# Performance work log

Measured on AMD Instinct MI355X. Metric: run time of the kernel, lower is better.

Reference implementation:

```python
import jax, jax.numpy as jnp
import numpy as np

B, N, E, H = 256, 128, 256, 256
C_CLIP = 10.0


def setup_inputs() -> dict:
    key = jax.random.key(0)
    ks = jax.random.split(key, 12)
    u = lambda k, shape, b: jax.random.uniform(k, shape, jnp.float32, -b, b)
    return {
        "low_context_vector": jax.random.normal(ks[0], (B, N, E), jnp.float32),
        "original_node": jax.random.uniform(ks[1], (B, N, 2), jnp.float32),
        "mask": jnp.zeros((B, N), jnp.int32),
        "id": 0,
        "low_init_w": u(ks[2], (2 * E,), 1.0),                      # uniform_(-1, 1)
        "W_hbar": u(ks[3], (E, E), 1.0 / np.sqrt(E)),
        "b_hbar": u(ks[4], (E,), 1.0 / np.sqrt(E)),
        "W_rest": u(ks[5], (2 * E, E), 1.0 / np.sqrt(2 * E)),
        "b_rest": u(ks[6], (E,), 1.0 / np.sqrt(2 * E)),
        "W_k": u(ks[7], (E, H), 1.0 / np.sqrt(E)),
        "b_k": u(ks[8], (H,), 1.0 / np.sqrt(E)),
        "W_q": u(ks[9], (E, H), 1.0 / np.sqrt(E)),
        "b_q": u(ks[10], (H,), 1.0 / np.sqrt(E)),
        "v": u(ks[11], (H,), 1.0 / np.sqrt(H)),
    }


def reference(low_context_vector, original_node, mask, id,
              low_init_w, W_hbar, b_hbar, W_rest, b_rest,
              W_k, b_k, W_q, b_q, v):
    lcv = low_context_vector
    b, n, e = lcv.shape
    barange = jnp.arange(b)
    # target side of the pointer is fixed across steps -> precompute keys
    keys = lcv @ W_k + b_k                                   # [B, N, H]
    h_bar = jnp.mean(lcv, axis=1) @ W_hbar + b_hbar          # [B, E]
    query0 = h_bar + (low_init_w @ W_rest + b_rest)          # [B, E] (broadcast)
    step_keys = jax.random.split(jax.random.key(42), n)

    def step(carry, xs):
        query, msk, init_h, cur_idx = carry
        i, k = xs
        q = query @ W_q + b_q                                # [B, H]
        u = jnp.tanh(keys + q[:, None, :]) @ v               # [B, N]
        logits = C_CLIP * jnp.tanh(u)
        logits = jnp.where(msk == 1, -jnp.inf, logits)       # masked_fill
        idx = jax.random.categorical(k, logits)              # Categorical sample
        idx = jnp.where((i == 0) & (id == 0), jnp.zeros_like(idx), idx)
        logp = jax.nn.log_softmax(logits)[barange, idx]      # [B]
        msk = msk.at[barange, idx].set(1)                    # Environment.update_state
        h = lcv[barange, idx]                                # gather current node emb
        init_h = jnp.where(i == 0, h, init_h)
        query = h_bar + (jnp.concatenate([init_h, h], axis=-1) @ W_rest + b_rest)
        cur = original_node[barange, cur_idx]                # [B, 2]
        nxt = original_node[barange, idx]
        r = jnp.linalg.norm(nxt - cur, axis=-1)              # [B]
        return (query, msk, init_h, idx), (logp, idx, r)

    carry0 = (query0, mask, jnp.zeros((b, e), lcv.dtype), jnp.zeros((b,), jnp.int64))
    (_, _, _, last_idx), (logps, idxs, rs) = jax.lax.scan(
        step, carry0, (jnp.arange(n), step_keys))
    init_node = original_node[:, :1, :]                      # current_idx starts at 0
    last_node = original_node[barange, last_idx][:, None, :]
    return (logps.T, idxs.T, init_node, last_node, rs.T)
```

## Files before the change

kernel.cpp:

```cpp
#include <hip/hip_runtime.h>
#include <stdint.h>
#include <math.h>

#define NN 128
#define EE 256
#define HH 256

#define OFF_LOGP 0
#define OFF_IDX  32768
#define OFF_INIT 65536
#define OFF_LAST 66048
#define OFF_RS   66560

#define KST  260
#define KST4 65

__device__ __forceinline__ uint32_t rotl32_(uint32_t x, int d){ return (x<<d)|(x>>(32-d)); }

__device__ __forceinline__ void tf2x32(uint32_t k0, uint32_t k1, uint32_t x0, uint32_t x1,
                                       uint32_t& o0, uint32_t& o1){
  uint32_t k2 = k0 ^ k1 ^ 0x1BD11BDAu;
  x0 += k0; x1 += k1;
#define TF_RND(r) { x0 += x1; x1 = rotl32_(x1,(r)); x1 ^= x0; }
  TF_RND(13) TF_RND(15) TF_RND(26) TF_RND(6)
  x0 += k1; x1 += k2 + 1u;
  TF_RND(17) TF_RND(29) TF_RND(16) TF_RND(24)
  x0 += k2; x1 += k0 + 2u;
  TF_RND(13) TF_RND(15) TF_RND(26) TF_RND(6)
  x0 += k0; x1 += k1 + 3u;
  TF_RND(17) TF_RND(29) TF_RND(16) TF_RND(24)
  x0 += k1; x1 += k2 + 4u;
  TF_RND(13) TF_RND(15) TF_RND(26) TF_RND(6)
  x0 += k2; x1 += k0 + 5u;
#undef TF_RND
  o0 = x0; o1 = x1;
}

__device__ __forceinline__ float fast_tanhf(float x){
  float ax = __builtin_fabsf(x);
  float E = __builtin_amdgcn_exp2f(ax * -2.885390081777927f);
  float num = 1.0f - E;
  float den = 1.0f + E;
  float inv = __builtin_amdgcn_rcpf(den);
  inv = fmaf(fmaf(-den, inv, 1.0f), inv, inv);
  float r = num * inv;
  r = fmaf(fmaf(-den, r, num), inv, r);
  return __builtin_copysignf(r, x);
}

__device__ __forceinline__ float tanh_pre(float xs){
  float E = __builtin_amdgcn_exp2f(xs);
  return fmaf(-2.0f, __builtin_amdgcn_rcpf(1.0f + E), 1.0f);
}

__device__ __forceinline__ float jax_gumbel(uint32_t k0, uint32_t k1, uint32_t t){
  uint32_t o0, o1, bits;
  tf2x32(k0, k1, 0u, t, o0, o1);
  bits = o0 ^ o1;
  float u = __uint_as_float((bits >> 9) | 0x3f800000u) - 1.0f;
  const float kTiny = 1.17549435e-38f;
  u = fmaxf(kTiny, u + kTiny);
  return -logf(-logf(u));
}

#define CMB_DPP(CTRL) { \
  float ny_ = __int_as_float(__builtin_amdgcn_mov_dpp(__float_as_int(y), (CTRL), 0xf, 0xf, false)); \
  int   nj_ = __builtin_amdgcn_mov_dpp(pj, (CTRL), 0xf, 0xf, false); \
  float ne_ = __int_as_float(__builtin_amdgcn_mov_dpp(__float_as_int(es), (CTRL), 0xf, 0xf, false)); \
  es += ne_; \
  if (ny_ > y || (ny_ == y && nj_ < pj)){ y = ny_; pj = nj_; } }
#define CMB_SWZ16() { \
  float ny_ = __int_as_float(__builtin_amdgcn_ds_swizzle(__float_as_int(y), 0x401F)); \
  int   nj_ = __builtin_amdgcn_ds_swizzle(pj, 0x401F); \
  float ne_ = __int_as_float(__builtin_amdgcn_ds_swizzle(__float_as_int(es), 0x401F)); \
  es += ne_; \
  if (ny_ > y || (ny_ == y && nj_ < pj)){ y = ny_; pj = nj_; } }
#define CMB_SHF32() { \
  float ny_ = __shfl_xor(y, 32); \
  int   nj_ = __shfl_xor(pj, 32); \
  float ne_ = __shfl_xor(es, 32); \
  es += ne_; \
  if (ny_ > y || (ny_ == y && nj_ < pj)){ y = ny_; pj = nj_; } }

__global__ __launch_bounds__(256) void k_pre(
    const float* __restrict__ liw, const float* __restrict__ Wr,
    const float* __restrict__ Wq, const float* __restrict__ lcv,
    const float* __restrict__ Whbar, const float* __restrict__ bhbar,
    const float* __restrict__ brest, const float* __restrict__ bq,
    float* __restrict__ c0, float* __restrict__ T1, float* __restrict__ base)
{
  __shared__ float sbuf[512];
  const int bid = blockIdx.x;
  const int t = threadIdx.x;
  if (bid == 0){
    float acc = 0.f;
    for (int k = 0; k < 2*EE; ++k) acc = fmaf(liw[k], Wr[(size_t)k*EE + t], acc);
    sbuf[t] = acc;
    __syncthreads();
    float c = 0.f;
    for (int e = 0; e < EE; ++e) c = fmaf(sbuf[e], Wq[(size_t)e*HH + t], c);
    c0[t] = c;
  } else if (bid <= 512){
    const int r = bid - 1;
    float acc = 0.f;
    for (int e = 0; e < EE; ++e) acc = fmaf(Wr[(size_t)r*EE + e], Wq[(size_t)e*HH + t], acc);
    T1[(size_t)r*HH + t] = acc;
  } else {
    const int b = bid - 513;
    float* sm  = sbuf;
    float* hb2 = sbuf + 256;
    float acc = 0.f;
    const float* p = lcv + (size_t)b*NN*EE + t;
    for (int n = 0; n < NN; ++n) acc += p[(size_t)n*EE];
    sm[t] = acc * 0.0078125f;
    __syncthreads();
    float a2 = 0.f;
    for (int e = 0; e < EE; ++e) a2 = fmaf(sm[e], Whbar[(size_t)e*EE + t], a2);
    hb2[t] = (a2 + bhbar[t]) + brest[t];
    __syncthreads();
    float a3 = 0.f;
    for (int e = 0; e < EE; ++e) a3 = fmaf(hb2[e], Wq[(size_t)e*HH + t], a3);
    base[(size_t)b*HH + t] = a3 + bq[t];
  }
}

__global__ __launch_bounds__(1024) void k_keysP2(
    const float* __restrict__ lcv, const float* __restrict__ Wk,
    const float* __restrict__ T1, const float* __restrict__ bk,
    const float* __restrict__ base, const float* __restrict__ c0,
    const float* __restrict__ vvec,
    float* __restrict__ keysg, float* __restrict__ P2g, float* __restrict__ ltab)
{
  const int b = blockIdx.x, tid = threadIdx.x, wid = tid >> 6, lane = tid & 63;
  __shared__ __align__(16) float sbuf[20992];
  __shared__ __align__(16) float q0s[EE];
  __shared__ __align__(16) float vs[EE];
  float* sA = sbuf;
  float* sW = sbuf + 4608;
  float* sT = sbuf + 12800;
  if (tid < 64){
    float4 bs = ((const float4*)(base + (size_t)b*HH))[tid];
    const float4 cc = ((const float4*)c0)[tid];
    bs.x += cc.x; bs.y += cc.y; bs.z += cc.z; bs.w += cc.w;
    ((float4*)q0s)[tid] = bs;
    ((float4*)vs)[tid]  = ((const float4*)vvec)[tid];
  }
  float4 kacc[8], p2acc[8];
  #pragma unroll
  for (int r = 0; r < 8; ++r){
    kacc[r]  = make_float4(0.f,0.f,0.f,0.f);
    p2acc[r] = make_float4(0.f,0.f,0.f,0.f);
  }
  for (int ch = 0; ch < 8; ++ch){
    const int e0 = ch << 5;
    __syncthreads();
    {
      const int r = tid >> 3, c = tid & 7;
      const float4 t = ((const float4*)(lcv + ((size_t)b*NN + r)*EE + e0))[c];
      ((float4*)sA)[r*9 + c] = t;
    }
    #pragma unroll
    for (int s = 0; s < 2; ++s){
      const int idx4 = s*1024 + tid;
      const int e = idx4 >> 6, c = idx4 & 63;
      ((float4*)sW)[idx4] = ((const float4*)(Wk + (size_t)(e0+e)*HH))[c];
      ((float4*)sT)[idx4] = ((const float4*)(T1 + (size_t)(EE+e0+e)*HH))[c];
    }
    __syncthreads();
    const float* aRow = sA + (wid << 3)*36;
    for (int e = 0; e < 32; ++e){
      const float4 wv = ((const float4*)sW)[(e<<6) + lane];
      const float4 tv = ((const float4*)sT)[(e<<6) + lane];
      #pragma unroll
      for (int r = 0; r < 8; ++r){
        const float av = aRow[r*36 + e];
        kacc[r].x = fmaf(av, wv.x, kacc[r].x);
        kacc[r].y = fmaf(av, wv.y, kacc[r].y);
        kacc[r].z = fmaf(av, wv.z, kacc[r].z);
        kacc[r].w = fmaf(av, wv.w, kacc[r].w);
        p2acc[r].x = fmaf(av, tv.x, p2acc[r].x);
        p2acc[r].y = fmaf(av, tv.y, p2acc[r].y);
        p2acc[r].z = fmaf(av, tv.z, p2acc[r].z);
        p2acc[r].w = fmaf(av, tv.w, p2acc[r].w);
      }
    }
  }
  const float4 bkv = ((const float4*)bk)[lane];
  const float4 qv0 = ((const float4*)q0s)[lane];
  const float4 vv0 = ((const float4*)vs)[lane];
  #pragma unroll
  for (int r = 0; r < 8; ++r){
    const int j = (wid << 3) + r;
    float4 kv = kacc[r];
    kv.x += bkv.x; kv.y += bkv.y; kv.z += bkv.z; kv.w += bkv.w;
    ((float4*)(keysg + ((size_t)b*NN + j)*EE))[lane] = kv;
    ((float4*)(P2g   + ((size_t)b*NN + j)*EE))[lane] = p2acc[r];
    float p = 0.f;
    p = fmaf(fast_tanhf(kv.x + qv0.x), vv0.x, p);
    p = fmaf(fast_tanhf(kv.y + qv0.y), vv0.y, p);
    p = fmaf(fast_tanhf(kv.z + qv0.z), vv0.z, p);
    p = fmaf(fast_tanhf(kv.w + qv0.w), vv0.w, p);
    #pragma unroll
    for (int off = 1; off < 64; off <<= 1) p += __shfl_xor(p, off);
    if (lane == 0) ltab[((size_t)b*129 + 128)*NN + j] = 10.0f * fast_tanhf(p);
  }
}

__global__ __launch_bounds__(256) void k_idx0qb(
    const float* __restrict__ ltab, const int* __restrict__ mask_in,
    const int* __restrict__ id_in, const float* __restrict__ lcv,
    const float* __restrict__ T1, const float* __restrict__ base,
    float* __restrict__ qb)
{
  const int b = blockIdx.x, t = threadIdx.x, lane = t & 63;
  __shared__ int idx_sh;
  if (t < 64){
    const float NEG_INF = -__builtin_huge_valf();
    float l0 = ltab[((size_t)b*129 + 128)*NN + lane];
    float l1 = ltab[((size_t)b*129 + 128)*NN + 64 + lane];
    if (mask_in[(size_t)b*NN + lane])      l0 = NEG_INF;
    if (mask_in[(size_t)b*NN + 64 + lane]) l1 = NEG_INF;
    uint32_t k0, k1; tf2x32(0u, 42u, 0u, 0u, k0, k1);
    const float g0 = jax_gumbel(k0, k1, (uint32_t)(b*NN + lane));
    const float g1 = jax_gumbel(k0, k1, (uint32_t)(b*NN + 64 + lane));
    float y = l0 + g0; int pj = lane;
    { float yb = l1 + g1; if (yb > y){ y = yb; pj = 64 + lane; } }
    float es = 0.f;
    CMB_DPP(0xB1); CMB_DPP(0x4E); CMB_DPP(0x124); CMB_DPP(0x128);
    CMB_SWZ16(); CMB_SHF32();
    int bi = pj;
    if (id_in[0] == 0) bi = 0;
    if (lane == 0) idx_sh = bi;
  }
  __syncthreads();
  const int i0 = idx_sh;
  const float* arow = lcv + ((size_t)b*NN + i0)*EE;
  float acc = 0.f;
  #pragma unroll 4
  for (int e = 0; e < EE; ++e) acc = fmaf(arow[e], T1[(size_t)e*HH + t], acc);
  qb[(size_t)b*HH + t] = base[(size_t)b*HH + t] + acc;
}

__global__ __launch_bounds__(256) void k_tab(
    const float* __restrict__ keysg, const float* __restrict__ P2g,
    const float* __restrict__ qb, const float* __restrict__ vvec,
    float* __restrict__ l_tab)
{
  const int b  = blockIdx.x >> 2;
  const int jt = blockIdx.x & 3;
  const int t = threadIdx.x;
  const float CSC = 2.885390081777927f;
  __shared__ __align__(16) float skeys[32*65*4];
  __shared__ __align__(16) float sQ2[32*65*4];
  __shared__ __align__(16) float sv[EE];
  __shared__ __align__(16) float sqbc[EE];

  #pragma unroll
  for (int k = 0; k < 8; ++k){
    const int idx4 = t + 256*k;
    const int row = idx4 >> 6, hc = idx4 & 63;
    float4 kv = ((const float4*)(keysg + ((size_t)b*NN + jt*32 + row)*EE))[hc];
    kv.x *= CSC; kv.y *= CSC; kv.z *= CSC; kv.w *= CSC;
    ((float4*)skeys)[row*65 + (hc ^ ((row >> 2) & 7))] = kv;
  }
  if (t < 64){
    ((float4*)sv)[t]  = ((const float4*)vvec)[t];
    float4 qv = ((const float4*)(qb + (size_t)b*HH))[t];
    qv.x *= CSC; qv.y *= CSC; qv.z *= CSC; qv.w *= CSC;
    ((float4*)sqbc)[t] = qv;
  }
  const int jq = t & 7;
  const int iq = t >> 3;

  float4 pr[8];
  #pragma unroll
  for (int k = 0; k < 8; ++k){
    const int idx4 = t + 256*k;
    const int row = idx4 >> 6, hc = idx4 & 63;
    pr[k] = ((const float4*)(P2g + ((size_t)b*NN + row)*EE))[hc];
  }

  for (int ib = 0; ib < 4; ++ib){
    __syncthreads();
    #pragma unroll
    for (int k = 0; k < 8; ++k){
      const int idx4 = t + 256*k;
      const int row = idx4 >> 6, hc = idx4 & 63;
      const float4 qv = ((const float4*)sqbc)[hc];
      float4 pv;
      pv.x = fmaf(pr[k].x, CSC, qv.x);
      pv.y = fmaf(pr[k].y, CSC, qv.y);
      pv.z = fmaf(pr[k].z, CSC, qv.z);
      pv.w = fmaf(pr[k].w, CSC, qv.w);
      ((float4*)sQ2)[row*65 + hc] = pv;
    }
    if (ib + 1 < 4){
      #pragma unroll
      for (int k = 0; k < 8; ++k){
        const int idx4 = t + 256*k;
        const int row = idx4 >> 6, hc = idx4 & 63;
        pr[k] = ((const float4*)(P2g + ((size_t)b*NN + (ib+1)*32 + row)*EE))[hc];
      }
    }
    __syncthreads();
    float a0 = 0.f, a1 = 0.f, a2 = 0.f, a3 = 0.f;
    #pragma unroll 2
    for (int hc = 0; hc < 64; ++hc){
      const float4 qv = ((const float4*)sQ2)[iq*65 + hc];
      const float4 vv = ((const float4*)sv)[hc];
      const int hx = hc ^ jq;
      const float4 k0 = ((const float4*)skeys)[(jq*4 + 0)*65 + hx];
      const float4 k1 = ((const float4*)skeys)[(jq*4 + 1)*65 + hx];
      const float4 k2 = ((const float4*)skeys)[(jq*4 + 2)*65 + hx];
      const float4 k3 = ((const float4*)skeys)[(jq*4 + 3)*65 + hx];
      a0 = fmaf(tanh_pre(k0.x + qv.x), vv.x, a0);
      a0 = fmaf(tanh_pre(k0.y + qv.y), vv.y, a0);
      a0 = fmaf(tanh_pre(k0.z + qv.z), vv.z, a0);
      a0 = fmaf(tanh_pre(k0.w + qv.w), vv.w, a0);
      a1 = fmaf(tanh_pre(k1.x + qv.x), vv.x, a1);
      a1 = fmaf(tanh_pre(k1.y + qv.y), vv.y, a1);
      a1 = fmaf(tanh_pre(k1.z + qv.z), vv.z, a1);
      a1 = fmaf(tanh_pre(k1.w + qv.w), vv.w, a1);
      a2 = fmaf(tanh_pre(k2.x + qv.x), vv.x, a2);
      a2 = fmaf(tanh_pre(k2.y + qv.y), vv.y, a2);
      a2 = fmaf(tanh_pre(k2.z + qv.z), vv.z, a2);
      a2 = fmaf(tanh_pre(k2.w + qv.w), vv.w, a2);
      a3 = fmaf(tanh_pre(k3.x + qv.x), vv.x, a3);
      a3 = fmaf(tanh_pre(k3.y + qv.y), vv.y, a3);
      a3 = fmaf(tanh_pre(k3.z + qv.z), vv.z, a3);
      a3 = fmaf(tanh_pre(k3.w + qv.w), vv.w, a3);
    }
    const int idx = ib*32 + iq;
    float* dst = l_tab + ((size_t)b*129 + idx)*NN + jt*32 + jq*4;
    dst[0] = 10.0f * fast_tanhf(a0);
    dst[1] = 10.0f * fast_tanhf(a1);
    dst[2] = 10.0f * fast_tanhf(a2);
    dst[3] = 10.0f * fast_tanhf(a3);
  }
}

__global__ __launch_bounds__(256) void k_seq(
    const float* __restrict__ l_tab, const float* __restrict__ onode,
    const int* __restrict__ mask_in, const int* __restrict__ id_in,
    float* __restrict__ out)
{
  const int b = blockIdx.x;
  const int tid = threadIdx.x;
  const int wid = tid >> 6;
  const int lane = tid & 63;
  __shared__ float l_s[129*NN];
  __shared__ float g_a[NN*NN];
  __shared__ float2 on_s[NN];
  __shared__ int   mask_s[NN];
  __shared__ uint32_t sk0[NN], sk1[NN];

  #pragma unroll
  for (int k = 0; k < 17; ++k){
    const int i4 = tid + 256*k;
    if (i4 < (129*NN)/4)
      ((float4*)l_s)[i4] = ((const float4*)(l_tab + (size_t)b*129*NN))[i4];
  }
  if (tid < NN){
    uint32_t o0, o1; tf2x32(0u, 42u, 0u, (uint32_t)tid, o0, o1);
    sk0[tid] = o0; sk1[tid] = o1;
    mask_s[tid] = mask_in[(size_t)b*NN + tid];
    on_s[tid] = ((const float2*)onode)[b*NN + tid];
  }
  __syncthreads();
  for (int k = 0; k < 64; ++k){
    const int p = tid + 256*k;
    const int i = p >> 7, j = p & 127;
    g_a[p] = jax_gumbel(sk0[i], sk1[i], (uint32_t)(b*NN + j));
  }
  __syncthreads();
  if (wid != 0) return;

  const int id0 = id_in[0];
  const float NEG_INF = -__builtin_huge_valf();
  if (lane == 0){
    out[OFF_INIT + 2*b]     = on_s[0].x;
    out[OFF_INIT + 2*b + 1] = on_s[0].y;
  }
  int prev = 128, cur = 0;
  for (int i = 0; i < NN; ++i){
    float l0 = l_s[prev*NN + lane];
    float l1 = l_s[prev*NN + 64 + lane];
    if (mask_s[lane])      l0 = NEG_INF;
    if (mask_s[64 + lane]) l1 = NEG_INF;
    float y = l0 + g_a[i*NN + lane]; int pj = lane;
    { float yb = l1 + g_a[i*NN + 64 + lane];
      if (yb > y){ y = yb; pj = 64 + lane; } }
    float es = __expf(l0) + __expf(l1);
    CMB_DPP(0xB1); CMB_DPP(0x4E); CMB_DPP(0x124); CMB_DPP(0x128);
    CMB_SWZ16(); CMB_SHF32();
    int bi = pj;
    if (i == 0 && id0 == 0) bi = 0;
    const float lsel = __shfl((bi & 64) ? l1 : l0, bi & 63);
    const float logp = lsel - __logf(es);
    if (lane == 0){
      out[OFF_LOGP + b*NN + i] = logp;
      out[OFF_IDX  + b*NN + i] = (float)bi;
      const float2 pc = on_s[cur];
      const float2 pn = on_s[bi];
      const float dx = pn.x - pc.x, dy = pn.y - pc.y;
      out[OFF_RS + b*NN + i] = sqrtf(dx*dx + dy*dy);
      if (i == NN-1){ out[OFF_LAST + 2*b] = pn.x; out[OFF_LAST + 2*b + 1] = pn.y; }
      mask_s[bi] = 1;
      cur = bi;
    }
    prev = bi;
  }
}

__global__ void k_tmp1(const float* __restrict__ liw, const float* __restrict__ Wr,
                       float* __restrict__ tmp1){
  int e = threadIdx.x;
  float acc = 0.f;
  for (int k = 0; k < 2*EE; ++k) acc = fmaf(liw[k], Wr[(size_t)k*EE + e], acc);
  tmp1[e] = acc;
}

__global__ void k_T1(const float* __restrict__ Wr, const float* __restrict__ Wq,
                     float* __restrict__ T1){
  int r = blockIdx.x, h = threadIdx.x;
  float acc = 0.f;
  for (int e = 0; e < EE; ++e) acc = fmaf(Wr[(size_t)r*EE + e], Wq[(size_t)e*HH + h], acc);
  T1[(size_t)r*HH + h] = acc;
}

__global__ void k_base(const float* __restrict__ lcv, const float* __restrict__ Whbar,
                       const float* __restrict__ bhbar, const float* __restrict__ brest,
                       const float* __restrict__ Wq, const float* __restrict__ bq,
                       float* __restrict__ base){
  __shared__ float sm[EE];
  __shared__ float hb2[EE];
  int b = blockIdx.x, t = threadIdx.x;
  float acc = 0.f;
  const float* p = lcv + (size_t)b*NN*EE + t;
  for (int n = 0; n < NN; ++n) acc += p[(size_t)n*EE];
  sm[t] = acc * 0.0078125f;
  __syncthreads();
  float a2 = 0.f;
  for (int e = 0; e < EE; ++e) a2 = fmaf(sm[e], Whbar[(size_t)e*EE + t], a2);
  hb2[t] = (a2 + bhbar[t]) + brest[t];
  __syncthreads();
  float a3 = 0.f;
  for (int e = 0; e < EE; ++e) a3 = fmaf(hb2[e], Wq[(size_t)e*HH + t], a3);
  base[(size_t)b*HH + t] = a3 + bq[t];
}

__global__ __launch_bounds__(1024, 4) void dec_main(
    const float* __restrict__ lcv, const float* __restrict__ onode,
    const int* __restrict__ mask_in, const int* __restrict__ id_in,
    const float* __restrict__ Wk, const float* __restrict__ bk,
    const float* __restrict__ vvec, const float* __restrict__ T1,
    const float* __restrict__ base, const float* __restrict__ tmp1,
    const float* __restrict__ Wq, float* __restrict__ out)
{
  const int b = blockIdx.x;
  const int tid = threadIdx.x;
  const int wid = tid >> 6;
  const int lane = tid & 63;

  __shared__ __align__(16) float keys_lds[NN*KST];
  __shared__ __align__(16) float q_s[272];
  __shared__ __align__(16) float base_s[HH];
  __shared__ __align__(16) float p1row[HH];
  __shared__ __align__(16) float2 on_s[NN];
  __shared__ float u_s[NN];
  __shared__ float g2_s[2][NN];
  __shared__ int act_s[NN];
  __shared__ int pos_s[NN];
  __shared__ int mask_s[NN];
  __shared__ uint32_t sk0[NN], sk1[NN];
  __shared__ int idx_sh, L_sh;

  const float NEG_INF = -__builtin_huge_valf();
  const int id0 = id_in[0];

  float4 kacc[8], p2acc[8];
  #pragma unroll
  for (int r = 0; r < 8; ++r){
    kacc[r]  = make_float4(0.f,0.f,0.f,0.f);
    p2acc[r] = make_float4(0.f,0.f,0.f,0.f);
  }
  {
    float* sA = keys_lds;
    float* sW = keys_lds + 4608;
    float* sT = keys_lds + 12800;
    for (int ch = 0; ch < 8; ++ch){
      const int e0 = ch << 5;
      __syncthreads();
      {
        const int r = tid >> 3, c = tid & 7;
        const float4 t = ((const float4*)(lcv + ((size_t)b*NN + r)*EE + e0))[c];
        ((float4*)sA)[r*9 + c] = t;
      }
      #pragma unroll
      for (int s = 0; s < 2; ++s){
        const int idx4 = s*1024 + tid;
        const int e = idx4 >> 6, c = idx4 & 63;
        ((float4*)sW)[idx4] = ((const float4*)(Wk + (size_t)(e0+e)*HH))[c];
        ((float4*)sT)[idx4] = ((const float4*)(T1 + (size_t)(EE+e0+e)*HH))[c];
      }
      __syncthreads();
      const float* aRow = sA + (wid << 3)*36;
      for (int e = 0; e < 32; ++e){
        const float4 wv = ((const float4*)sW)[(e<<6) + lane];
        const float4 tv = ((const float4*)sT)[(e<<6) + lane];
        #pragma unroll
        for (int r = 0; r < 8; ++r){
          const float av = aRow[r*36 + e];
          kacc[r].x = fmaf(av, wv.x, kacc[r].x);
          kacc[r].y = fmaf(av, wv.y, kacc[r].y);
          kacc[r].z = fmaf(av, wv.z, kacc[r].z);
          kacc[r].w = fmaf(av, wv.w, kacc[r].w);
          p2acc[r].x = fmaf(av, tv.x, p2acc[r].x);
          p2acc[r].y = fmaf(av, tv.y, p2acc[r].y);
          p2acc[r].z = fmaf(av, tv.z, p2acc[r].z);
          p2acc[r].w = fmaf(av, tv.w, p2acc[r].w);
        }
      }
    }
  }
  __syncthreads();
  {
    const float4 bkv = ((const float4*)bk)[lane];
    const int sphys = ((lane >> 4) << 4) | ((lane & 15) ^ (lane >> 4));
    #pragma unroll
    for (int r = 0; r < 8; ++r){
      const int j = (wid << 3) + r;
      float4 kv = kacc[r];
      kv.x += bkv.x; kv.y += bkv.y; kv.z += bkv.z; kv.w += bkv.w;
      ((float4*)keys_lds)[j*KST4 + sphys] = kv;
    }
  }

  const int grp = tid & 3;
  const int aslot = tid >> 2;

  float4 vreg[16];
  #pragma unroll
  for (int c = 0; c < 16; ++c) vreg[c] = ((const float4*)vvec)[(grp << 4) + c];

  if (tid < HH){
    const float bs = base[(size_t)b*HH + tid];
    base_s[tid] = bs;
    float c0v = 0.f;
    for (int e = 0; e < EE; ++e) c0v = fmaf(tmp1[e], Wq[(size_t)e*HH + tid], c0v);
    q_s[(tid>>6)*68 + (tid&63)] = bs + c0v;
  } else if (tid < HH + NN){
    const int j = tid - HH;
    mask_s[j] = mask_in[(size_t)b*NN + j];
    uint32_t o0,o1; tf2x32(0u, 42u, 0u, (uint32_t)j, o0, o1);
    sk0[j] = o0; sk1[j] = o1;
  } else if (tid == HH + NN){
    out[OFF_INIT + 2*b]     = onode[(size_t)b*NN*2 + 0];
    out[OFF_INIT + 2*b + 1] = onode[(size_t)b*NN*2 + 1];
  } else if (tid >= 512 && tid < 512 + NN){
    on_s[tid - 512] = ((const float2*)onode)[b*NN + (tid - 512)];
  }
  __syncthreads();
  if (tid == 0){
    int L = 0;
    for (int j = 0; j < NN; ++j){
      if (mask_s[j] == 0){ act_s[L] = j; pos_s[j] = L; ++L; }
    }
    L_sh = L;
  }
  if (wid == 15){
    g2_s[0][lane]      = jax_gumbel(sk0[0], sk1[0], (uint32_t)(b*NN + lane));
    g2_s[0][64 + lane] = jax_gumbel(sk0[0], sk1[0], (uint32_t)(b*NN + 64 + lane));
  }

  int cur = 0;

  for (int i = 0; i < NN; ++i){
    __syncthreads();
    const int L = L_sh;
    if (aslot < L){
      const int j = act_s[aslot];
      const int kb4 = j*KST4 + (grp << 4);
      const int qb4 = grp*17;
      float s = 0.f;
      #pragma unroll
      for (int c4 = 0; c4 < 4; ++c4){
        float th[16];
        #pragma unroll
        for (int cc = 0; cc < 4; ++cc){
          const int c = c4*4 + cc;
          const float4 kv = ((const float4*)keys_lds)[kb4 + (c ^ grp)];
          const float4 qv = ((const float4*)q_s)[qb4 + c];
          th[4*cc+0] = fast_tanhf(kv.x + qv.x);
          th[4*cc+1] = fast_tanhf(kv.y + qv.y);
          th[4*cc+2] = fast_tanhf(kv.z + qv.z);
          th[4*cc+3] = fast_tanhf(kv.w + qv.w);
        }
        #pragma unroll
        for (int cc = 0; cc < 4; ++cc){
          const float4 vv = vreg[c4*4 + cc];
          s = fmaf(th[4*cc+0], vv.x, s);
          s = fmaf(th[4*cc+1], vv.y, s);
          s = fmaf(th[4*cc+2], vv.z, s);
          s = fmaf(th[4*cc+3], vv.w, s);
        }
      }
      s += __shfl_xor(s, 1);
      s += __shfl_xor(s, 2);
      if (grp == 0) u_s[j] = s;
    } else if (wid == 15 && i + 1 < NN){
      const int nb = (i + 1) & 1;
      g2_s[nb][lane]      = jax_gumbel(sk0[i+1], sk1[i+1], (uint32_t)(b*NN + lane));
      g2_s[nb][64 + lane] = jax_gumbel(sk0[i+1], sk1[i+1], (uint32_t)(b*NN + 64 + lane));
    }
    __syncthreads();
    float l0 = 0.f, l1 = 0.f; int bi = 0;
    if (wid == 0){
      l0 = 10.0f * fast_tanhf(u_s[lane]);
      l1 = 10.0f * fast_tanhf(u_s[64 + lane]);
      if (mask_s[lane])      l0 = NEG_INF;
      if (mask_s[64 + lane]) l1 = NEG_INF;
      const float y0 = l0 + g2_s[i & 1][lane];
      const float y1 = l1 + g2_s[i & 1][64 + lane];
      float bv;
      if (y1 > y0){ bv = y1; bi = 64 + lane; } else { bv = y0; bi = lane; }
      #pragma unroll
      for (int off = 1; off < 64; off <<= 1){
        const float ov = __shfl_xor(bv, off);
        const int   oi = __shfl_xor(bi, off);
        if (ov > bv || (ov == bv && oi < bi)){ bv = ov; bi = oi; }
      }
      if (i == 0 && id0 == 0) bi = 0;
      if (lane == 0) idx_sh = bi;
    }
    __syncthreads();
    const int idx = idx_sh;
    if (i == 0){
      if (tid < HH){
        const float* arow = lcv + ((size_t)b*NN + idx)*EE;
        float acc = 0.f;
        for (int e = 0; e < EE; ++e) acc = fmaf(arow[e], T1[(size_t)e*HH + tid], acc);
        p1row[tid] = acc;
      }
      __syncthreads();
    }
    if (wid == (idx >> 3)){
      const int r2 = idx & 7;
      float4 pp;
      switch (r2){
        case 0: pp = p2acc[0]; break;
        case 1: pp = p2acc[1]; break;
        case 2: pp = p2acc[2]; break;
        case 3: pp = p2acc[3]; break;
        case 4: pp = p2acc[4]; break;
        case 5: pp = p2acc[5]; break;
        case 6: pp = p2acc[6]; break;
        default: pp = p2acc[7]; break;
      }
      const float4 b4 = ((const float4*)base_s)[lane];
      const float4 p4 = ((const float4*)p1row)[lane];
      float4 nq;
      nq.x = (b4.x + p4.x) + pp.x;
      nq.y = (b4.y + p4.y) + pp.y;
      nq.z = (b4.z + p4.z) + pp.z;
      nq.w = (b4.w + p4.w) + pp.w;
      ((float4*)q_s)[((lane >> 4)*17) + (lane & 15)] = nq;
    }
    if (wid == 0){
      float es = __expf(l0) + __expf(l1);
      #pragma unroll
      for (int off = 1; off < 64; off <<= 1) es += __shfl_xor(es, off);
      const float lown = (bi >= 64) ? l1 : l0;
      const float lsel = __shfl(lown, bi & 63);
      const float logp = lsel - __logf(es);
      if (lane == 0){
        out[OFF_LOGP + b*NN + i] = logp;
        out[OFF_IDX  + b*NN + i] = (float)bi;
        const float2 pc = on_s[cur];
        const float2 pn = on_s[bi];
        const float dx = pn.x - pc.x, dy = pn.y - pc.y;
        out[OFF_RS + b*NN + i] = sqrtf(dx*dx + dy*dy);
        if (i == NN-1){ out[OFF_LAST + 2*b] = pn.x; out[OFF_LAST + 2*b + 1] = pn.y; }
        cur = bi;
        if (mask_s[bi] == 0){
          mask_s[bi] = 1;
          const int p = pos_s[bi];
          const int Lm = L_sh - 1;
          const int last = act_s[Lm];
          act_s[p] = last;
          pos_s[last] = p;
          L_sh = Lm;
        }
      }
    }
  }
}

extern "C" void kernel_launch(void* const* d_in, const int* in_sizes, int n_in,
                              void* d_out, int out_size, void* d_ws, size_t ws_size,
                              hipStream_t stream){
  const float* lcv   = (const float*)d_in[0];
  const float* onode = (const float*)d_in[1];
  const int*   mask  = (const int*)d_in[2];
  const int*   id    = (const int*)d_in[3];
  const float* liw   = (const float*)d_in[4];
  const float* Whbar = (const float*)d_in[5];
  const float* bhbar = (const float*)d_in[6];
  const float* Wrest = (const float*)d_in[7];
  const float* brest = (const float*)d_in[8];
  const float* Wk    = (const float*)d_in[9];
  const float* bk    = (const float*)d_in[10];
  const float* Wq    = (const float*)d_in[11];
  const float* bq    = (const float*)d_in[12];
  const float* vv    = (const float*)d_in[13];

  float* ws  = (float*)d_ws;
  float* out = (float*)d_out;

  const size_t NEED_BYTES = 21267200ull * 4ull;

  if (ws_size >= NEED_BYTES){
    float* T1   = ws;
    float* base = ws + 131072;
    float* c0   = ws + 196864;
    float* qb   = ws + 197120;
    float* keys = ws + 262912;
    float* P2   = ws + 8651520;
    float* ltab = ws + 17040128;

    hipLaunchKernelGGL(k_pre,    dim3(769),  dim3(256),  0, stream,
                       liw, Wrest, Wq, lcv, Whbar, bhbar, brest, bq, c0, T1, base);
    hipLaunchKernelGGL(k_keysP2, dim3(256),  dim3(1024), 0, stream,
                       lcv, Wk, T1, bk, base, c0, vv, keys, P2, ltab);
    hipLaunchKernelGGL(k_idx0qb, dim3(256),  dim3(256),  0, stream,
                       ltab, mask, id, lcv, T1, base, qb);
    hipLaunchKernelGGL(k_tab,    dim3(1024), dim3(256),  0, stream, keys, P2, qb, vv, ltab);
    hipLaunchKernelGGL(k_seq,    dim3(256),  dim3(256),  0, stream, ltab, onode, mask, id, out);
  } else {
    float* T1   = ws;
    float* base = ws + 131072;
    float* tmp1 = ws + 196608;

    hipLaunchKernelGGL(k_tmp1, dim3(1),   dim3(256), 0, stream, liw, Wrest, tmp1);
    hipLaunchKernelGGL(k_T1,   dim3(512), dim3(256), 0, stream, Wrest, Wq, T1);
    hipLaunchKernelGGL(k_base, dim3(256), dim3(256), 0, stream, lcv, Whbar, bhbar, brest, Wq, bq, base);
    hipLaunchKernelGGL(dec_main, dim3(256), dim3(1024), 0, stream,
                       lcv, onode, mask, id, Wk, bk, vv, T1, base, tmp1, Wq, out);
  }
}
```

Measured before the change: 453.1 us.

## Precompute Gumbel table in prologue, fuse idx0 into keys kernel, retile table kernel

```diff
diff --git a/kernel.cpp b/kernel.cpp
--- a/kernel.cpp
+++ b/kernel.cpp
@@ -87,9 +87,11 @@
     const float* __restrict__ Wq, const float* __restrict__ lcv,
     const float* __restrict__ Whbar, const float* __restrict__ bhbar,
     const float* __restrict__ brest, const float* __restrict__ bq,
-    float* __restrict__ c0, float* __restrict__ T1, float* __restrict__ base)
+    float* __restrict__ c0, float* __restrict__ T1, float* __restrict__ base,
+    float* __restrict__ g_tab)
 {
   __shared__ float sbuf[512];
+  __shared__ uint32_t gk0[NN], gk1[NN];
   const int bid = blockIdx.x;
   const int t = threadIdx.x;
   if (bid == 0){
@@ -105,7 +107,7 @@
     float acc = 0.f;
     for (int e = 0; e < EE; ++e) acc = fmaf(Wr[(size_t)r*EE + e], Wq[(size_t)e*HH + t], acc);
     T1[(size_t)r*HH + t] = acc;
-  } else {
+  } else if (bid <= 768){
     const int b = bid - 513;
     float* sm  = sbuf;
     float* hb2 = sbuf + 256;
@@ -121,6 +123,18 @@
     float a3 = 0.f;
     for (int e = 0; e < EE; ++e) a3 = fmaf(hb2[e], Wq[(size_t)e*HH + t], a3);
     base[(size_t)b*HH + t] = a3 + bq[t];
+  } else {
+    const int b2 = bid - 769;
+    if (t < NN){
+      uint32_t o0, o1; tf2x32(0u, 42u, 0u, (uint32_t)t, o0, o1);
+      gk0[t] = o0; gk1[t] = o1;
+    }
+    __syncthreads();
+    for (int k = 0; k < 64; ++k){
+      const int p = t + 256*k;
+      const int i = p >> 7, j = p & 127;
+      g_tab[(size_t)b2*16384 + p] = jax_gumbel(gk0[i], gk1[i], (uint32_t)(b2*NN + j));
+    }
   }
 }
 
@@ -128,13 +142,17 @@
     const float* __restrict__ lcv, const float* __restrict__ Wk,
     const float* __restrict__ T1, const float* __restrict__ bk,
     const float* __restrict__ base, const float* __restrict__ c0,
-    const float* __restrict__ vvec,
-    float* __restrict__ keysg, float* __restrict__ P2g, float* __restrict__ ltab)
+    const float* __restrict__ vvec, const int* __restrict__ mask_in,
+    const int* __restrict__ id_in,
+    float* __restrict__ keysg, float* __restrict__ P2g, float* __restrict__ ltab,
+    float* __restrict__ qbg)
 {
   const int b = blockIdx.x, tid = threadIdx.x, wid = tid >> 6, lane = tid & 63;
   __shared__ __align__(16) float sbuf[20992];
   __shared__ __align__(16) float q0s[EE];
   __shared__ __align__(16) float vs[EE];
+  __shared__ float l0s[NN];
+  __shared__ int idx_sh;
   float* sA = sbuf;
   float* sW = sbuf + 4608;
   float* sT = sbuf + 12800;
@@ -202,22 +220,17 @@
     p = fmaf(fast_tanhf(kv.w + qv0.w), vv0.w, p);
     #pragma unroll
     for (int off = 1; off < 64; off <<= 1) p += __shfl_xor(p, off);
-    if (lane == 0) ltab[((size_t)b*129 + 128)*NN + j] = 10.0f * fast_tanhf(p);
-  }
-}
-
-__global__ __launch_bounds__(256) void k_idx0qb(
-    const float* __restrict__ ltab, const int* __restrict__ mask_in,
-    const int* __restrict__ id_in, const float* __restrict__ lcv,
-    const float* __restrict__ T1, const float* __restrict__ base,
-    float* __restrict__ qb)
-{
-  const int b = blockIdx.x, t = threadIdx.x, lane = t & 63;
-  __shared__ int idx_sh;
-  if (t < 64){
+    if (lane == 0){
+      const float lv = 10.0f * fast_tanhf(p);
+      ltab[((size_t)b*129 + 128)*NN + j] = lv;
+      l0s[j] = lv;
+    }
+  }
+  __syncthreads();
+  if (tid < 64){
     const float NEG_INF = -__builtin_huge_valf();
-    float l0 = ltab[((size_t)b*129 + 128)*NN + lane];
-    float l1 = ltab[((size_t)b*129 + 128)*NN + 64 + lane];
+    float l0 = l0s[lane];
+    float l1 = l0s[64 + lane];
     if (mask_in[(size_t)b*NN + lane])      l0 = NEG_INF;
     if (mask_in[(size_t)b*NN + 64 + lane]) l1 = NEG_INF;
     uint32_t k0, k1; tf2x32(0u, 42u, 0u, 0u, k0, k1);
@@ -233,12 +246,13 @@
     if (lane == 0) idx_sh = bi;
   }
   __syncthreads();
-  const int i0 = idx_sh;
-  const float* arow = lcv + ((size_t)b*NN + i0)*EE;
-  float acc = 0.f;
-  #pragma unroll 4
-  for (int e = 0; e < EE; ++e) acc = fmaf(arow[e], T1[(size_t)e*HH + t], acc);
-  qb[(size_t)b*HH + t] = base[(size_t)b*HH + t] + acc;
+  if (tid < HH){
+    const float* arow = lcv + ((size_t)b*NN + idx_sh)*EE;
+    float acc = 0.f;
+    #pragma unroll 4
+    for (int e = 0; e < EE; ++e) acc = fmaf(arow[e], T1[(size_t)e*HH + tid], acc);
+    qbg[(size_t)b*HH + tid] = base[(size_t)b*HH + tid] + acc;
+  }
 }
 
 __global__ __launch_bounds__(256) void k_tab(
@@ -251,7 +265,7 @@
   const int t = threadIdx.x;
   const float CSC = 2.885390081777927f;
   __shared__ __align__(16) float skeys[32*65*4];
-  __shared__ __align__(16) float sQ2[32*65*4];
+  __shared__ __align__(16) float sQ2[16*65*4];
   __shared__ __align__(16) float sv[EE];
   __shared__ __align__(16) float sqbc[EE];
 
@@ -261,7 +275,7 @@
     const int row = idx4 >> 6, hc = idx4 & 63;
     float4 kv = ((const float4*)(keysg + ((size_t)b*NN + jt*32 + row)*EE))[hc];
     kv.x *= CSC; kv.y *= CSC; kv.z *= CSC; kv.w *= CSC;
-    ((float4*)skeys)[row*65 + (hc ^ ((row >> 2) & 7))] = kv;
+    ((float4*)skeys)[row*65 + (hc ^ ((row >> 1) & 7))] = kv;
   }
   if (t < 64){
     ((float4*)sv)[t]  = ((const float4*)vvec)[t];
@@ -269,21 +283,24 @@
     qv.x *= CSC; qv.y *= CSC; qv.z *= CSC; qv.w *= CSC;
     ((float4*)sqbc)[t] = qv;
   }
-  const int jq = t & 7;
-  const int iq = t >> 3;
-
-  float4 pr[8];
+  const int iq = t >> 4;
+  const int jq = (t >> 1) & 7;
+  const int s  = t & 1;
+  const int jp = jq*4 + s*2;
+  const int swz = (jp >> 1) & 7;
+
+  float4 pr[4];
   #pragma unroll
-  for (int k = 0; k < 8; ++k){
+  for (int k = 0; k < 4; ++k){
     const int idx4 = t + 256*k;
     const int row = idx4 >> 6, hc = idx4 & 63;
     pr[k] = ((const float4*)(P2g + ((size_t)b*NN + row)*EE))[hc];
   }
 
-  for (int ib = 0; ib < 4; ++ib){
+  for (int ib = 0; ib < 8; ++ib){
     __syncthreads();
     #pragma unroll
-    for (int k = 0; k < 8; ++k){
+    for (int k = 0; k < 4; ++k){
       const int idx4 = t + 256*k;
       const int row = idx4 >> 6, hc = idx4 & 63;
       const float4 qv = ((const float4*)sqbc)[hc];
@@ -294,25 +311,26 @@
       pv.w = fmaf(pr[k].w, CSC, qv.w);
       ((float4*)sQ2)[row*65 + hc] = pv;
     }
-    if (ib + 1 < 4){
+    if (ib + 1 < 8){
       #pragma unroll
-      for (int k = 0; k < 8; ++k){
+      for (int k = 0; k < 4; ++k){
         const int idx4 = t + 256*k;
         const int row = idx4 >> 6, hc = idx4 & 63;
-        pr[k] = ((const float4*)(P2g + ((size_t)b*NN + (ib+1)*32 + row)*EE))[hc];
-      }
-    }
-    __syncthreads();
-    float a0 = 0.f, a1 = 0.f, a2 = 0.f, a3 = 0.f;
-    #pragma unroll 2
+        pr[k] = ((const float4*)(P2g + ((size_t)b*NN + (ib+1)*16 + row)*EE))[hc];
+      }
+    }
+    __syncthreads();
+    float a0 = 0.f, a1 = 0.f;
+    const float4* krow0 = (const float4*)skeys + (size_t)jp*65;
+    const float4* krow1 = (const float4*)skeys + (size_t)(jp + 1)*65;
+    const float4* qrow  = (const float4*)sQ2   + (size_t)iq*65;
+    #pragma unroll 16
     for (int hc = 0; hc < 64; ++hc){
-      const float4 qv = ((const float4*)sQ2)[iq*65 + hc];
+      const float4 qv = qrow[hc];
       const float4 vv = ((const float4*)sv)[hc];
-      const int hx = hc ^ jq;
-      const float4 k0 = ((const float4*)skeys)[(jq*4 + 0)*65 + hx];
-      const float4 k1 = ((const float4*)skeys)[(jq*4 + 1)*65 + hx];
-      const float4 k2 = ((const float4*)skeys)[(jq*4 + 2)*65 + hx];
-      const float4 k3 = ((const float4*)skeys)[(jq*4 + 3)*65 + hx];
+      const int hx = hc ^ swz;
+      const float4 k0 = krow0[hx];
+      const float4 k1 = krow1[hx];
       a0 = fmaf(tanh_pre(k0.x + qv.x), vv.x, a0);
       a0 = fmaf(tanh_pre(k0.y + qv.y), vv.y, a0);
       a0 = fmaf(tanh_pre(k0.z + qv.z), vv.z, a0);
@@ -321,28 +339,18 @@
       a1 = fmaf(tanh_pre(k1.y + qv.y), vv.y, a1);
       a1 = fmaf(tanh_pre(k1.z + qv.z), vv.z, a1);
       a1 = fmaf(tanh_pre(k1.w + qv.w), vv.w, a1);
-      a2 = fmaf(tanh_pre(k2.x + qv.x), vv.x, a2);
-      a2 = fmaf(tanh_pre(k2.y + qv.y), vv.y, a2);
-      a2 = fmaf(tanh_pre(k2.z + qv.z), vv.z, a2);
-      a2 = fmaf(tanh_pre(k2.w + qv.w), vv.w, a2);
-      a3 = fmaf(tanh_pre(k3.x + qv.x), vv.x, a3);
-      a3 = fmaf(tanh_pre(k3.y + qv.y), vv.y, a3);
-      a3 = fmaf(tanh_pre(k3.z + qv.z), vv.z, a3);
-      a3 = fmaf(tanh_pre(k3.w + qv.w), vv.w, a3);
-    }
-    const int idx = ib*32 + iq;
-    float* dst = l_tab + ((size_t)b*129 + idx)*NN + jt*32 + jq*4;
+    }
+    const int idx = ib*16 + iq;
+    float* dst = l_tab + ((size_t)b*129 + idx)*NN + jt*32 + jp;
     dst[0] = 10.0f * fast_tanhf(a0);
     dst[1] = 10.0f * fast_tanhf(a1);
-    dst[2] = 10.0f * fast_tanhf(a2);
-    dst[3] = 10.0f * fast_tanhf(a3);
   }
 }
 
 __global__ __launch_bounds__(256) void k_seq(
     const float* __restrict__ l_tab, const float* __restrict__ onode,
     const int* __restrict__ mask_in, const int* __restrict__ id_in,
-    float* __restrict__ out)
+    const float* __restrict__ g_tab, float* __restrict__ out)
 {
   const int b = blockIdx.x;
   const int tid = threadIdx.x;
@@ -361,18 +369,27 @@
       ((float4*)l_s)[i4] = ((const float4*)(l_tab + (size_t)b*129*NN))[i4];
   }
   if (tid < NN){
-    uint32_t o0, o1; tf2x32(0u, 42u, 0u, (uint32_t)tid, o0, o1);
-    sk0[tid] = o0; sk1[tid] = o1;
     mask_s[tid] = mask_in[(size_t)b*NN + tid];
     on_s[tid] = ((const float2*)onode)[b*NN + tid];
-  }
-  __syncthreads();
-  for (int k = 0; k < 64; ++k){
-    const int p = tid + 256*k;
-    const int i = p >> 7, j = p & 127;
-    g_a[p] = jax_gumbel(sk0[i], sk1[i], (uint32_t)(b*NN + j));
-  }
-  __syncthreads();
+    if (!g_tab){
+      uint32_t o0, o1; tf2x32(0u, 42u, 0u, (uint32_t)tid, o0, o1);
+      sk0[tid] = o0; sk1[tid] = o1;
+    }
+  }
+  if (g_tab){
+    #pragma unroll
+    for (int k = 0; k < 16; ++k)
+      ((float4*)g_a)[tid + 256*k] = ((const float4*)(g_tab + (size_t)b*16384))[tid + 256*k];
+    __syncthreads();
+  } else {
+    __syncthreads();
+    for (int k = 0; k < 64; ++k){
+      const int p = tid + 256*k;
+      const int i = p >> 7, j = p & 127;
+      g_a[p] = jax_gumbel(sk0[i], sk1[i], (uint32_t)(b*NN + j));
+    }
+    __syncthreads();
+  }
   if (wid != 0) return;
 
   const int id0 = id_in[0];
@@ -717,9 +734,10 @@
   float* ws  = (float*)d_ws;
   float* out = (float*)d_out;
 
-  const size_t NEED_BYTES = 21267200ull * 4ull;
-
-  if (ws_size >= NEED_BYTES){
+  const size_t NEED_BASE = 21267200ull * 4ull;
+  const size_t NEED_FULL = 25461504ull * 4ull;
+
+  if (ws_size >= NEED_BASE){
     float* T1   = ws;
     float* base = ws + 131072;
     float* c0   = ws + 196864;
@@ -727,15 +745,14 @@
     float* keys = ws + 262912;
     float* P2   = ws + 8651520;
     float* ltab = ws + 17040128;
-
-    hipLaunchKernelGGL(k_pre,    dim3(769),  dim3(256),  0, stream,
-                       liw, Wrest, Wq, lcv, Whbar, bhbar, brest, bq, c0, T1, base);
-    hipLaunchKernelGGL(k_keysP2, dim3(256),  dim3(1024), 0, stream,
-                       lcv, Wk, T1, bk, base, c0, vv, keys, P2, ltab);
-    hipLaunchKernelGGL(k_idx0qb, dim3(256),  dim3(256),  0, stream,
-                       ltab, mask, id, lcv, T1, base, qb);
-    hipLaunchKernelGGL(k_tab,    dim3(1024), dim3(256),  0, stream, keys, P2, qb, vv, ltab);
-    hipLaunchKernelGGL(k_seq,    dim3(256),  dim3(256),  0, stream, ltab, onode, mask, id, out);
+    float* gtab = (ws_size >= NEED_FULL) ? (ws + 21267200) : (float*)nullptr;
+
+    hipLaunchKernelGGL(k_pre, dim3(gtab ? 1025 : 769), dim3(256), 0, stream,
+                       liw, Wrest, Wq, lcv, Whbar, bhbar, brest, bq, c0, T1, base, gtab);
+    hipLaunchKernelGGL(k_keysP2, dim3(256), dim3(1024), 0, stream,
+                       lcv, Wk, T1, bk, base, c0, vv, mask, id, keys, P2, ltab, qb);
+    hipLaunchKernelGGL(k_tab, dim3(1024), dim3(256), 0, stream, keys, P2, qb, vv, ltab);
+    hipLaunchKernelGGL(k_seq, dim3(256), dim3(256), 0, stream, ltab, onode, mask, id, gtab, out);
   } else {
     float* T1   = ws;
     float* base = ws + 131072;
```

Result: no change. 460.4 us (+1.6%).
